# Performance work log

Measured on AMD Instinct MI355X. Metric: run time of the kernel, lower is better.

## Reference

```python
import jax, jax.numpy as jnp
import numpy as np

B, S, D = 2, 2048, 1024
H, DH = 16, 64
NEG = -1e9


def setup_inputs() -> dict:
    key = jax.random.key(0)
    ks = jax.random.split(key, 4)
    hidden_states = jax.random.normal(ks[0], (B, S, D), dtype=jnp.float32)
    # additive causal mask: 0 where allowed, -1e9 where masked
    causal = jnp.tril(jnp.ones((S, S), dtype=bool))
    attention_mask = jnp.where(causal, 0.0, NEG).astype(jnp.float32)[None, None]
    Wqkv = jax.random.normal(ks[1], (D, 3 * H * DH), dtype=jnp.float32) * (1.0 / np.sqrt(D))
    bqkv = jnp.zeros((3 * H * DH,), dtype=jnp.float32)
    Wproj = jax.random.normal(ks[2], (H * DH, D), dtype=jnp.float32) * (1.0 / np.sqrt(H * DH))
    bproj = jnp.zeros((D,), dtype=jnp.float32)
    return {"hidden_states": hidden_states, "attention_mask": attention_mask,
            "Wqkv": Wqkv, "bqkv": bqkv, "Wproj": Wproj, "bproj": bproj}


def reference(hidden_states, attention_mask, Wqkv, bqkv, Wproj, bproj):
    b, s, _ = hidden_states.shape
    scale = 1.0 / np.sqrt(DH)
    qkv = hidden_states @ Wqkv + bqkv                      # [b, s, 3*H*DH]
    q, k, v = jnp.split(qkv, 3, axis=-1)
    # [b, s, H*DH] -> [b, H, s, DH]
    def split_heads(x):
        return x.reshape(b, s, H, DH).transpose(0, 2, 1, 3)
    q, k, v = split_heads(q), split_heads(k), split_heads(v)
    scores = jnp.einsum('bhqd,bhkd->bhqk', q, k) * scale   # [b, H, s, s]
    scores = scores + attention_mask
    probs = jax.nn.softmax(scores, axis=-1)
    attn = jnp.einsum('bhqk,bhkd->bhqd', probs, v)         # [b, H, s, DH]
    attn = attn.transpose(0, 2, 1, 3).reshape(b, s, H * DH)
    out = attn @ Wproj + bproj                             # [b, s, D]
    return out
```

## Files before the change

### kernel.cpp

```cpp
#include <hip/hip_runtime.h>
#include <hip/hip_bf16.h>
#include <stdint.h>

#define B_ 2
#define S_ 2048
#define D_ 1024
#define H_ 16
#define DH_ 64
#define M_ 4096
#define LOG2E 1.44269504088896340736f

typedef __attribute__((ext_vector_type(8))) short short8;
typedef __attribute__((ext_vector_type(4))) float f32x4;
typedef __attribute__((ext_vector_type(16))) float f32x16;

__device__ __forceinline__ unsigned short f2bf(float f) {
  __hip_bfloat16 h = __float2bfloat16(f);
  union { __hip_bfloat16 h; unsigned short u; } cv;
  cv.h = h;
  return cv.u;
}

__device__ __forceinline__ unsigned int pack_bf(float lo, float hi2) {
  union { __hip_bfloat162 h; unsigned int u; } cv;
  cv.h = __float22bfloat162_rn(make_float2(lo, hi2));
  return cv.u;
}

__device__ __forceinline__ void gll16(const void* g, void* l) {
  __builtin_amdgcn_global_load_lds(
      (__attribute__((address_space(1))) void*)(g),
      (__attribute__((address_space(3))) void*)(l), 16, 0, 0);
}

__global__ __launch_bounds__(256) void k_prep(const float* __restrict__ hs,
                                              const float* __restrict__ Wqkv,
                                              const float* __restrict__ Wproj,
                                              unsigned short* __restrict__ hid,
                                              unsigned short* __restrict__ wqkvT,
                                              unsigned short* __restrict__ wprT) {
  __shared__ unsigned short tile[32][33];
  const int id = blockIdx.x;
  if (id < 4096) {
    const int i = id * 256 + threadIdx.x;
    float4 v = reinterpret_cast<const float4*>(hs)[i];
    ushort4 o;
    o.x = f2bf(v.x); o.y = f2bf(v.y); o.z = f2bf(v.z); o.w = f2bf(v.w);
    reinterpret_cast<ushort4*>(hid)[i] = o;
    return;
  }
  const float* W;
  unsigned short* WT;
  int N, i;
  if (id < 7168) { i = id - 4096; W = Wqkv; WT = wqkvT; N = 3072; }
  else           { i = id - 7168; W = Wproj; WT = wprT; N = 1024; }
  const int nb = (N == 3072) ? 96 : 32;
  const int n0 = (i % nb) * 32, k0 = (i / nb) * 32;
  const int tx = threadIdx.x & 31, ty = threadIdx.x >> 5;
#pragma unroll
  for (int j = 0; j < 4; j++) {
    int k = ty + j * 8;
    tile[k][tx] = f2bf(W[(long)(k0 + k) * N + n0 + tx]);
  }
  __syncthreads();
#pragma unroll
  for (int j = 0; j < 4; j++) {
    int n = ty + j * 8;
    WT[(long)(n0 + n) * 1024 + k0 + tx] = tile[tx][n];
  }
}

template <int MODE, int BN>
__global__ __launch_bounds__(256) void k_gemm(
    const unsigned short* __restrict__ A,
    const unsigned short* __restrict__ BT,
    const float* __restrict__ bias,
    void* __restrict__ out0,
    unsigned short* __restrict__ outk,
    unsigned short* __restrict__ outv,
    int M, int N, int K) {
  constexpr int JN = BN / 32;
  __shared__ __align__(16) unsigned short lds_a[2][128 * 32];
  __shared__ __align__(16) unsigned short lds_b[2][BN * 32];
  const int t = threadIdx.x;
  const int w = t >> 6, l = t & 63;
  const int g = l >> 4, x = l & 15;
  const int wr = w >> 1, wc = w & 1;
  const long m0 = (long)blockIdx.x * 128, n0 = (long)blockIdx.y * BN;

  f32x4 acc[4][JN];
#pragma unroll
  for (int i = 0; i < 4; i++)
#pragma unroll
    for (int j = 0; j < JN; j++) acc[i][j] = (f32x4){0.f, 0.f, 0.f, 0.f};

  const unsigned short* ga = A + (m0 + 16 * w + (l >> 2)) * (long)K + (l & 3) * 8;
  const unsigned short* gb = BT + (n0 + 16 * w + (l >> 2)) * (long)K + (l & 3) * 8;

  auto stage = [&](int nb, int k0) {
    unsigned short* la = lds_a[nb] + w * 512;
    unsigned short* lb = lds_b[nb] + w * 512;
    gll16(ga + k0, la);
    gll16(ga + k0 + 64 * (long)K, la + 2048);
    gll16(gb + k0, lb);
    if (BN == 128) gll16(gb + k0 + 64 * (long)K, lb + 2048);
  };

  stage(0, 0);
  asm volatile("s_waitcnt vmcnt(0)" ::: "memory");
  __syncthreads();

  const int nit = K >> 5;
  for (int it = 0; it < nit; it++) {
    const int cur = it & 1;
    if (it + 1 < nit) stage(cur ^ 1, (it + 1) << 5);
    short8 af[4], bfr[JN];
#pragma unroll
    for (int i = 0; i < 4; i++)
      af[i] = *reinterpret_cast<const short8*>(
          lds_a[cur] + (wr * 64 + i * 16 + x) * 32 + g * 8);
#pragma unroll
    for (int j = 0; j < JN; j++)
      bfr[j] = *reinterpret_cast<const short8*>(
          lds_b[cur] + (wc * (BN / 2) + j * 16 + x) * 32 + g * 8);
#pragma unroll
    for (int i = 0; i < 4; i++)
#pragma unroll
      for (int j = 0; j < JN; j++)
        acc[i][j] = __builtin_amdgcn_mfma_f32_16x16x32_bf16(af[i], bfr[j], acc[i][j], 0, 0, 0);
    asm volatile("s_waitcnt vmcnt(0)" ::: "memory");
    __syncthreads();
  }

#pragma unroll
  for (int i = 0; i < 4; i++) {
#pragma unroll
    for (int j = 0; j < JN; j++) {
#pragma unroll
      for (int r = 0; r < 4; r++) {
        const long m = m0 + wr * 64 + i * 16 + 4 * g + r;
        const long n = n0 + wc * (BN / 2) + j * 16 + x;
        float v = acc[i][j][r] + bias[n];
        if (MODE == 1) {
          ((float*)out0)[m * N + n] = v;
        } else {
          const int b = (int)(m >> 11), s = (int)(m & 2047);
          const int which = (int)(n >> 10);
          const int rem = (int)(n & 1023);
          const int h = rem >> 6, d = rem & 63;
          const long idx = (((long)(b * H_ + h)) * S_ + s) * DH_ + d;
          unsigned short bv = f2bf(v);
          if (which == 0) ((unsigned short*)out0)[idx] = bv;
          else if (which == 1) outk[idx] = bv;
          else outv[idx] = bv;
        }
      }
    }
  }
}

__global__ __launch_bounds__(256) void k_tr_v(const unsigned short* __restrict__ v,
                                              unsigned short* __restrict__ vt) {
  __shared__ __align__(16) unsigned short tile[64][72];
  const int bh = blockIdx.y;
  const int s0 = blockIdx.x * 64;
  const int t = threadIdx.x;
  const int r = t >> 2;
  const int c = (t & 3) * 16;
  const unsigned short* src = v + ((long)bh * S_ + s0 + r) * DH_ + c;
  *reinterpret_cast<short8*>(&tile[r][c]) = *reinterpret_cast<const short8*>(src);
  *reinterpret_cast<short8*>(&tile[r][c + 8]) = *reinterpret_cast<const short8*>(src + 8);
  __syncthreads();
  unsigned short* dst = vt + ((long)bh * DH_ + r) * S_ + s0 + c;
#pragma unroll
  for (int jj = 0; jj < 2; jj++) {
    short8 o;
#pragma unroll
    for (int j = 0; j < 8; j++) o[j] = (short)tile[c + jj * 8 + j][r];
    *reinterpret_cast<short8*>(dst + jj * 8) = o;
  }
}

__global__ __launch_bounds__(256, 1) void k_attn(const unsigned short* __restrict__ qb_,
                                                 const unsigned short* __restrict__ kb,
                                                 const unsigned short* __restrict__ vt,
                                                 unsigned short* __restrict__ attn_out) {
  __shared__ __align__(16) unsigned short lds_k[2][8192];
  __shared__ __align__(16) unsigned short lds_v[2][8192];

  const int t0_ = threadIdx.x;
  const int w = t0_ >> 6, l = t0_ & 63;
  const int q32 = l & 31, hi = l >> 5;
  const int r7 = q32 & 7;
  const int r15 = q32 & 15;
  const int lr = l >> 3, sch = (l & 7) ^ lr;
  const int lv4 = l >> 4;

  const int id = blockIdx.x;
  const int xcd = id & 7, slot = id >> 3;
  const int bh = xcd + 8 * (slot >> 4);
  const int craw = slot & 15;
  const int qc = (slot & 32) ? craw : (15 - craw);

  const int b = bh >> 4, h = bh & 15;
  const long kvbase = (long)bh * S_ * DH_;
  const long vtbase = (long)bh * DH_ * S_;
  const float SC = 0.125f * LOG2E;

  const int q0w = qc * 128 + 32 * w;
  const int qg = q0w + q32;
  const int nt = qc + 1;

  const unsigned short* kbb = kb + kvbase;
  const unsigned short* vtb = vt + vtbase;

  auto stage = [&](int nb, int kv0) {
#pragma unroll
    for (int i = 0; i < 4; i++) {
      const int R0 = 32 * w + 8 * i;
      gll16(kbb + (long)(kv0 + R0 + lr) * 64 + sch * 8, &lds_k[nb][R0 * 64]);
      const int V0 = 16 * w + 4 * i;
      const int svch = (l & 15) ^ (4 * i + lv4);
      gll16(vtb + (long)(V0 + lv4) * S_ + kv0 + svch * 8, &lds_v[nb][V0 * 128]);
    }
  };

  short8 qf[4];
#pragma unroll
  for (int f = 0; f < 4; f++)
    qf[f] = *reinterpret_cast<const short8*>(qb_ + kvbase + (long)qg * DH_ + 16 * f + 8 * hi);

  stage(0, 0);

  f32x16 oacc[2];
#pragma unroll
  for (int dt = 0; dt < 2; dt++)
#pragma unroll
    for (int r = 0; r < 16; r++) oacc[dt][r] = 0.f;
  float m = -1.0e30f, lown = 0.f;

  asm volatile("s_waitcnt vmcnt(0)" ::: "memory");
  __syncthreads();

  for (int tt = 0; tt < nt; tt++) {
    const int kv0 = tt << 7;
    if (tt + 1 < nt) stage((tt + 1) & 1, kv0 + 128);

    const unsigned short* lk = lds_k[tt & 1];
    const unsigned short* lv = lds_v[tt & 1];

    float p[64];
    const bool diag = (tt == nt - 1);
#pragma unroll
    for (int ks = 0; ks < 4; ks++) {
      f32x16 sa;
#pragma unroll
      for (int r = 0; r < 16; r++) sa[r] = 0.f;
#pragma unroll
      for (int f = 0; f < 4; f++) {
        short8 kf = *reinterpret_cast<const short8*>(
            lk + (32 * ks + q32) * 64 + (((2 * f + hi) ^ r7) << 3));
        sa = __builtin_amdgcn_mfma_f32_32x32x16_bf16(kf, qf[f], sa, 0, 0, 0);
      }
#pragma unroll
      for (int r = 0; r < 16; r++) {
        float s = sa[r] * SC;
        if (diag) {
          const int kvg = kv0 + 32 * ks + (r & 3) + 8 * (r >> 2) + 4 * hi;
          if (kvg > qg) s = -1.0e30f;
        }
        p[16 * ks + r] = s;
      }
    }

    float mx[16];
#pragma unroll
    for (int r = 0; r < 16; r++)
      mx[r] = fmaxf(fmaxf(p[r], p[r + 16]), fmaxf(p[r + 32], p[r + 48]));
#pragma unroll
    for (int st = 8; st >= 1; st >>= 1)
#pragma unroll
      for (int r = 0; r < 8; r++)
        if (r < st) mx[r] = fmaxf(mx[r], mx[r + st]);
    float pmax = fmaxf(mx[0], __shfl_xor(mx[0], 32, 64));

    if (__any(pmax > m + 8.0f)) {
      const float mn = fmaxf(m, pmax);
      const float fsc = exp2f(m - mn);
      m = mn;
      lown *= fsc;
#pragma unroll
      for (int r = 0; r < 16; r++) {
        const int rr = (r & 3) + 8 * (r >> 2) + 4 * hi;
        const float fr = __int_as_float(
            __builtin_amdgcn_ds_bpermute(rr << 2, __float_as_int(fsc)));
        oacc[0][r] *= fr;
        oacc[1][r] *= fr;
      }
    }

#pragma unroll
    for (int i = 0; i < 64; i++) p[i] = exp2f(p[i] - m);

    float sm[16];
#pragma unroll
    for (int r = 0; r < 16; r++)
      sm[r] = (p[r] + p[r + 16]) + (p[r + 32] + p[r + 48]);
#pragma unroll
    for (int st = 8; st >= 1; st >>= 1)
#pragma unroll
      for (int r = 0; r < 8; r++)
        if (r < st) sm[r] += sm[r + st];
    lown += sm[0];

#pragma unroll
    for (int s4 = 0; s4 < 8; s4++) {
      const int bse = 8 * s4;
      unsigned int t0p = pack_bf(p[bse + 0], p[bse + 1]);
      unsigned int t1p = pack_bf(p[bse + 2], p[bse + 3]);
      unsigned int t2p = pack_bf(p[bse + 4], p[bse + 5]);
      unsigned int t3p = pack_bf(p[bse + 6], p[bse + 7]);
      unsigned int s0 = hi ? t0p : t2p;
      unsigned int s1 = hi ? t1p : t3p;
      unsigned int x0 = __shfl_xor(s0, 32, 64);
      unsigned int x1 = __shfl_xor(s1, 32, 64);
      union { unsigned int u[4]; short8 s8; } pa;
      pa.u[0] = hi ? x0 : t0p;
      pa.u[1] = hi ? x1 : t1p;
      pa.u[2] = hi ? t2p : x0;
      pa.u[3] = hi ? t3p : x1;
#pragma unroll
      for (int dt = 0; dt < 2; dt++) {
        short8 vf = *reinterpret_cast<const short8*>(
            lv + (32 * dt + q32) * 128 + (((2 * s4 + hi) ^ r15) << 3));
        oacc[dt] = __builtin_amdgcn_mfma_f32_32x32x16_bf16(pa.s8, vf, oacc[dt], 0, 0, 0);
      }
    }

    asm volatile("s_waitcnt vmcnt(0)" ::: "memory");
    __syncthreads();
  }

  const float lt = lown + __shfl_xor(lown, 32, 64);
  const float linv = 1.0f / lt;
#pragma unroll
  for (int r = 0; r < 16; r++) {
    const int rr = (r & 3) + 8 * (r >> 2) + 4 * hi;
    const float li = __int_as_float(
        __builtin_amdgcn_ds_bpermute(rr << 2, __float_as_int(linv)));
    const long row = (long)b * S_ + q0w + rr;
#pragma unroll
    for (int dt = 0; dt < 2; dt++)
      attn_out[row * (H_ * DH_) + h * DH_ + 32 * dt + q32] = f2bf(oacc[dt][r] * li);
  }
}

extern "C" void kernel_launch(void* const* d_in, const int* in_sizes, int n_in,
                              void* d_out, int out_size, void* d_ws, size_t ws_size,
                              hipStream_t stream) {
  (void)in_sizes; (void)n_in; (void)out_size; (void)ws_size;
  const float* hs    = (const float*)d_in[0];
  const float* Wqkv  = (const float*)d_in[2];
  const float* bqkv  = (const float*)d_in[3];
  const float* Wproj = (const float*)d_in[4];
  const float* bproj = (const float*)d_in[5];
  float* out = (float*)d_out;

  unsigned short* ws    = (unsigned short*)d_ws;
  unsigned short* hid   = ws;
  unsigned short* wqkvT = hid + 4194304;
  unsigned short* wprT  = wqkvT + 3145728;
  unsigned short* q_b   = wprT + 1048576;
  unsigned short* k_b   = q_b + 4194304;
  unsigned short* v_b   = k_b + 4194304;
  unsigned short* vt_b  = v_b + 4194304;
  unsigned short* ao    = vt_b + 4194304;

  k_prep<<<8192, 256, 0, stream>>>(hs, Wqkv, Wproj, hid, wqkvT, wprT);
  k_gemm<0, 128><<<dim3(32, 24), 256, 0, stream>>>(hid, wqkvT, bqkv, (void*)q_b, k_b, v_b,
                                                   4096, 3072, 1024);
  k_tr_v<<<dim3(32, 32), 256, 0, stream>>>(v_b, vt_b);
  k_attn<<<512, 256, 0, stream>>>(q_b, k_b, vt_b, ao);
  k_gemm<1, 64><<<dim3(32, 16), 256, 0, stream>>>(ao, wprT, bproj, (void*)out, nullptr, nullptr,
                                                  4096, 1024, 1024);
}
```

Measured before the change: 212.8 us.

## Split attention KV range across two wave groups and pair causal chunks per block

The attention kernel now uses 512-thread blocks where two 4-wave groups each process alternating KV tiles for the same 128-query chunk, then merge their partial softmax states through LDS. Each block handles a pair of query chunks (pr and 15-pr) so every block gets equal causal work, and the grid shrinks to 256 blocks. This aims to fix load imbalance from the causal triangle and add parallelism within a chunk. In exchange it costs extra LDS, a combine step with bf16-rounded partial outputs, and more barriers.

```diff
diff --git a/kernel.cpp b/kernel.cpp
--- a/kernel.cpp
+++ b/kernel.cpp
@@ -19,6 +19,10 @@
   union { __hip_bfloat16 h; unsigned short u; } cv;
   cv.h = h;
   return cv.u;
+}
+
+__device__ __forceinline__ float bf2f(unsigned short u) {
+  union { uint32_t u; float f; } x; x.u = (uint32_t)u << 16; return x.f;
 }
 
 __device__ __forceinline__ unsigned int pack_bf(float lo, float hi2) {
@@ -181,177 +185,214 @@
   }
 }
 
-__global__ __launch_bounds__(256, 1) void k_attn(const unsigned short* __restrict__ qb_,
+__global__ __launch_bounds__(512, 2) void k_attn(const unsigned short* __restrict__ qb_,
                                                  const unsigned short* __restrict__ kb,
                                                  const unsigned short* __restrict__ vt,
                                                  unsigned short* __restrict__ attn_out) {
-  __shared__ __align__(16) unsigned short lds_k[2][8192];
-  __shared__ __align__(16) unsigned short lds_v[2][8192];
+  __shared__ __align__(16) unsigned short lds_k[2][2][8192];
+  __shared__ __align__(16) unsigned short lds_v[2][2][8192];
+  __shared__ float cmb_m[256], cmb_l[256];
+  __shared__ unsigned int cmb_o[256][16];
 
   const int t0_ = threadIdx.x;
-  const int w = t0_ >> 6, l = t0_ & 63;
+  const int w = t0_ >> 6;
+  const int grp = w >> 2, wi = w & 3;
+  const int l = t0_ & 63;
   const int q32 = l & 31, hi = l >> 5;
   const int r7 = q32 & 7;
   const int r15 = q32 & 15;
   const int lr = l >> 3, sch = (l & 7) ^ lr;
   const int lv4 = l >> 4;
+  const int slot = wi * 64 + l;
 
   const int id = blockIdx.x;
-  const int xcd = id & 7, slot = id >> 3;
-  const int bh = xcd + 8 * (slot >> 4);
-  const int craw = slot & 15;
-  const int qc = (slot & 32) ? craw : (15 - craw);
+  const int xcd = id & 7, sl2 = id >> 3;
+  const int bh = 4 * xcd + (sl2 & 3);
+  const int pr = sl2 >> 2;
 
   const int b = bh >> 4, h = bh & 15;
   const long kvbase = (long)bh * S_ * DH_;
   const long vtbase = (long)bh * DH_ * S_;
   const float SC = 0.125f * LOG2E;
 
-  const int q0w = qc * 128 + 32 * w;
-  const int qg = q0w + q32;
-  const int nt = qc + 1;
-
   const unsigned short* kbb = kb + kvbase;
   const unsigned short* vtb = vt + vtbase;
 
-  auto stage = [&](int nb, int kv0) {
+  auto stage = [&](int buf, int kv0) {
 #pragma unroll
     for (int i = 0; i < 4; i++) {
-      const int R0 = 32 * w + 8 * i;
-      gll16(kbb + (long)(kv0 + R0 + lr) * 64 + sch * 8, &lds_k[nb][R0 * 64]);
-      const int V0 = 16 * w + 4 * i;
+      const int R0 = 32 * wi + 8 * i;
+      gll16(kbb + (long)(kv0 + R0 + lr) * 64 + sch * 8, &lds_k[grp][buf][R0 * 64]);
+      const int V0 = 16 * wi + 4 * i;
       const int svch = (l & 15) ^ (4 * i + lv4);
-      gll16(vtb + (long)(V0 + lv4) * S_ + kv0 + svch * 8, &lds_v[nb][V0 * 128]);
+      gll16(vtb + (long)(V0 + lv4) * S_ + kv0 + svch * 8, &lds_v[grp][buf][V0 * 128]);
     }
   };
 
-  short8 qf[4];
-#pragma unroll
-  for (int f = 0; f < 4; f++)
-    qf[f] = *reinterpret_cast<const short8*>(qb_ + kvbase + (long)qg * DH_ + 16 * f + 8 * hi);
-
-  stage(0, 0);
-
-  f32x16 oacc[2];
-#pragma unroll
-  for (int dt = 0; dt < 2; dt++)
-#pragma unroll
-    for (int r = 0; r < 16; r++) oacc[dt][r] = 0.f;
-  float m = -1.0e30f, lown = 0.f;
-
-  asm volatile("s_waitcnt vmcnt(0)" ::: "memory");
-  __syncthreads();
-
-  for (int tt = 0; tt < nt; tt++) {
-    const int kv0 = tt << 7;
-    if (tt + 1 < nt) stage((tt + 1) & 1, kv0 + 128);
-
-    const unsigned short* lk = lds_k[tt & 1];
-    const unsigned short* lv = lds_v[tt & 1];
-
-    float p[64];
-    const bool diag = (tt == nt - 1);
-#pragma unroll
-    for (int ks = 0; ks < 4; ks++) {
-      f32x16 sa;
-#pragma unroll
-      for (int r = 0; r < 16; r++) sa[r] = 0.f;
-#pragma unroll
-      for (int f = 0; f < 4; f++) {
-        short8 kf = *reinterpret_cast<const short8*>(
-            lk + (32 * ks + q32) * 64 + (((2 * f + hi) ^ r7) << 3));
-        sa = __builtin_amdgcn_mfma_f32_32x32x16_bf16(kf, qf[f], sa, 0, 0, 0);
+#pragma unroll 1
+  for (int ch = 0; ch < 2; ch++) {
+    const int qc = ch ? (15 - pr) : pr;
+    const int ntot = qc + 1;
+    const int N = (ntot + 1) >> 1;
+    const int ng = (ntot + (grp == 0 ? 1 : 0)) >> 1;
+
+    const int q0w = qc * 128 + 32 * wi;
+    const int qg = q0w + q32;
+
+    short8 qf[4];
+#pragma unroll
+    for (int f = 0; f < 4; f++)
+      qf[f] = *reinterpret_cast<const short8*>(
+          qb_ + kvbase + (long)qg * DH_ + 16 * f + 8 * hi);
+
+    f32x16 oacc[2];
+#pragma unroll
+    for (int dt = 0; dt < 2; dt++)
+#pragma unroll
+      for (int r = 0; r < 16; r++) oacc[dt][r] = 0.f;
+    float m = -1.0e30f, lown = 0.f;
+
+    if (ng > 0) stage(0, grp << 7);
+    asm volatile("s_waitcnt vmcnt(0)" ::: "memory");
+    __syncthreads();
+
+    for (int s = 0; s < N; s++) {
+      const int tile = grp + 2 * s;
+      if (s + 1 < ng) stage((s + 1) & 1, (grp + 2 * (s + 1)) << 7);
+      if (s < ng) {
+        const int kv0 = tile << 7;
+        const unsigned short* lk = lds_k[grp][s & 1];
+        const unsigned short* lv = lds_v[grp][s & 1];
+        const bool diag = (tile == qc);
+
+        float p[64];
+#pragma unroll
+        for (int ks = 0; ks < 4; ks++) {
+          f32x16 sa;
+#pragma unroll
+          for (int r = 0; r < 16; r++) sa[r] = 0.f;
+#pragma unroll
+          for (int f = 0; f < 4; f++) {
+            short8 kf = *reinterpret_cast<const short8*>(
+                lk + (32 * ks + q32) * 64 + (((2 * f + hi) ^ r7) << 3));
+            sa = __builtin_amdgcn_mfma_f32_32x32x16_bf16(kf, qf[f], sa, 0, 0, 0);
+          }
+#pragma unroll
+          for (int r = 0; r < 16; r++) {
+            float s2 = sa[r] * SC;
+            if (diag) {
+              const int kvg = kv0 + 32 * ks + (r & 3) + 8 * (r >> 2) + 4 * hi;
+              if (kvg > qg) s2 = -1.0e30f;
+            }
+            p[16 * ks + r] = s2;
+          }
+        }
+
+        float mx[16];
+#pragma unroll
+        for (int r = 0; r < 16; r++)
+          mx[r] = fmaxf(fmaxf(p[r], p[r + 16]), fmaxf(p[r + 32], p[r + 48]));
+#pragma unroll
+        for (int st = 8; st >= 1; st >>= 1)
+#pragma unroll
+          for (int r = 0; r < 8; r++)
+            if (r < st) mx[r] = fmaxf(mx[r], mx[r + st]);
+        float pmax = fmaxf(mx[0], __shfl_xor(mx[0], 32, 64));
+
+        if (__any(pmax > m + 8.0f)) {
+          const float mn = fmaxf(m, pmax);
+          const float fsc = exp2f(m - mn);
+          m = mn;
+          lown *= fsc;
+#pragma unroll
+          for (int r = 0; r < 16; r++) {
+            const int rr = (r & 3) + 8 * (r >> 2) + 4 * hi;
+            const float fr = __int_as_float(
+                __builtin_amdgcn_ds_bpermute(rr << 2, __float_as_int(fsc)));
+            oacc[0][r] *= fr;
+            oacc[1][r] *= fr;
+          }
+        }
+
+#pragma unroll
+        for (int i = 0; i < 64; i++) p[i] = exp2f(p[i] - m);
+
+        float sm[16];
+#pragma unroll
+        for (int r = 0; r < 16; r++)
+          sm[r] = (p[r] + p[r + 16]) + (p[r + 32] + p[r + 48]);
+#pragma unroll
+        for (int st = 8; st >= 1; st >>= 1)
+#pragma unroll
+          for (int r = 0; r < 8; r++)
+            if (r < st) sm[r] += sm[r + st];
+        lown += sm[0];
+
+#pragma unroll
+        for (int s4 = 0; s4 < 8; s4++) {
+          const int bse = 8 * s4;
+          unsigned int t0p = pack_bf(p[bse + 0], p[bse + 1]);
+          unsigned int t1p = pack_bf(p[bse + 2], p[bse + 3]);
+          unsigned int t2p = pack_bf(p[bse + 4], p[bse + 5]);
+          unsigned int t3p = pack_bf(p[bse + 6], p[bse + 7]);
+          unsigned int s0 = hi ? t0p : t2p;
+          unsigned int s1 = hi ? t1p : t3p;
+          unsigned int x0 = __shfl_xor(s0, 32, 64);
+          unsigned int x1 = __shfl_xor(s1, 32, 64);
+          union { unsigned int u[4]; short8 s8; } pa;
+          pa.u[0] = hi ? x0 : t0p;
+          pa.u[1] = hi ? x1 : t1p;
+          pa.u[2] = hi ? t2p : x0;
+          pa.u[3] = hi ? t3p : x1;
+#pragma unroll
+          for (int dt = 0; dt < 2; dt++) {
+            short8 vf = *reinterpret_cast<const short8*>(
+                lv + (32 * dt + q32) * 128 + (((2 * s4 + hi) ^ r15) << 3));
+            oacc[dt] = __builtin_amdgcn_mfma_f32_32x32x16_bf16(pa.s8, vf, oacc[dt], 0, 0, 0);
+          }
+        }
       }
+      asm volatile("s_waitcnt vmcnt(0)" ::: "memory");
+      __syncthreads();
+    }
+
+    if (grp == 1) {
+      const float lt1 = lown + __shfl_xor(lown, 32, 64);
+      cmb_m[slot] = m;
+      cmb_l[slot] = lt1;
+#pragma unroll
+      for (int dt = 0; dt < 2; dt++)
+#pragma unroll
+        for (int i = 0; i < 8; i++)
+          cmb_o[slot][dt * 8 + i] = pack_bf(oacc[dt][2 * i], oacc[dt][2 * i + 1]);
+    }
+    __syncthreads();
+    if (grp == 0) {
+      const float lt0 = lown + __shfl_xor(lown, 32, 64);
+      const float m1 = cmb_m[slot], l1c = cmb_l[slot];
+      const float ms = fmaxf(m, m1);
+      const float w0 = exp2f(m - ms), w1 = exp2f(m1 - ms);
+      const float linv = 1.0f / (w0 * lt0 + w1 * l1c);
 #pragma unroll
       for (int r = 0; r < 16; r++) {
-        float s = sa[r] * SC;
-        if (diag) {
-          const int kvg = kv0 + 32 * ks + (r & 3) + 8 * (r >> 2) + 4 * hi;
-          if (kvg > qg) s = -1.0e30f;
+        const int rr = (r & 3) + 8 * (r >> 2) + 4 * hi;
+        const float w0r = __int_as_float(
+            __builtin_amdgcn_ds_bpermute(rr << 2, __float_as_int(w0)));
+        const float w1r = __int_as_float(
+            __builtin_amdgcn_ds_bpermute(rr << 2, __float_as_int(w1)));
+        const float lir = __int_as_float(
+            __builtin_amdgcn_ds_bpermute(rr << 2, __float_as_int(linv)));
+        const long row = (long)b * S_ + q0w + rr;
+#pragma unroll
+        for (int dt = 0; dt < 2; dt++) {
+          const unsigned int wd = cmb_o[slot][dt * 8 + (r >> 1)];
+          const float o1 = bf2f((unsigned short)((r & 1) ? (wd >> 16) : (wd & 0xffffu)));
+          attn_out[row * (H_ * DH_) + h * DH_ + 32 * dt + q32] =
+              f2bf((w0r * oacc[dt][r] + w1r * o1) * lir);
         }
-        p[16 * ks + r] = s;
       }
     }
-
-    float mx[16];
-#pragma unroll
-    for (int r = 0; r < 16; r++)
-      mx[r] = fmaxf(fmaxf(p[r], p[r + 16]), fmaxf(p[r + 32], p[r + 48]));
-#pragma unroll
-    for (int st = 8; st >= 1; st >>= 1)
-#pragma unroll
-      for (int r = 0; r < 8; r++)
-        if (r < st) mx[r] = fmaxf(mx[r], mx[r + st]);
-    float pmax = fmaxf(mx[0], __shfl_xor(mx[0], 32, 64));
-
-    if (__any(pmax > m + 8.0f)) {
-      const float mn = fmaxf(m, pmax);
-      const float fsc = exp2f(m - mn);
-      m = mn;
-      lown *= fsc;
-#pragma unroll
-      for (int r = 0; r < 16; r++) {
-        const int rr = (r & 3) + 8 * (r >> 2) + 4 * hi;
-        const float fr = __int_as_float(
-            __builtin_amdgcn_ds_bpermute(rr << 2, __float_as_int(fsc)));
-        oacc[0][r] *= fr;
-        oacc[1][r] *= fr;
-      }
-    }
-
-#pragma unroll
-    for (int i = 0; i < 64; i++) p[i] = exp2f(p[i] - m);
-
-    float sm[16];
-#pragma unroll
-    for (int r = 0; r < 16; r++)
-      sm[r] = (p[r] + p[r + 16]) + (p[r + 32] + p[r + 48]);
-#pragma unroll
-    for (int st = 8; st >= 1; st >>= 1)
-#pragma unroll
-      for (int r = 0; r < 8; r++)
-        if (r < st) sm[r] += sm[r + st];
-    lown += sm[0];
-
-#pragma unroll
-    for (int s4 = 0; s4 < 8; s4++) {
-      const int bse = 8 * s4;
-      unsigned int t0p = pack_bf(p[bse + 0], p[bse + 1]);
-      unsigned int t1p = pack_bf(p[bse + 2], p[bse + 3]);
-      unsigned int t2p = pack_bf(p[bse + 4], p[bse + 5]);
-      unsigned int t3p = pack_bf(p[bse + 6], p[bse + 7]);
-      unsigned int s0 = hi ? t0p : t2p;
-      unsigned int s1 = hi ? t1p : t3p;
-      unsigned int x0 = __shfl_xor(s0, 32, 64);
-      unsigned int x1 = __shfl_xor(s1, 32, 64);
-      union { unsigned int u[4]; short8 s8; } pa;
-      pa.u[0] = hi ? x0 : t0p;
-      pa.u[1] = hi ? x1 : t1p;
-      pa.u[2] = hi ? t2p : x0;
-      pa.u[3] = hi ? t3p : x1;
-#pragma unroll
-      for (int dt = 0; dt < 2; dt++) {
-        short8 vf = *reinterpret_cast<const short8*>(
-            lv + (32 * dt + q32) * 128 + (((2 * s4 + hi) ^ r15) << 3));
-        oacc[dt] = __builtin_amdgcn_mfma_f32_32x32x16_bf16(pa.s8, vf, oacc[dt], 0, 0, 0);
-      }
-    }
-
-    asm volatile("s_waitcnt vmcnt(0)" ::: "memory");
     __syncthreads();
-  }
-
-  const float lt = lown + __shfl_xor(lown, 32, 64);
-  const float linv = 1.0f / lt;
-#pragma unroll
-  for (int r = 0; r < 16; r++) {
-    const int rr = (r & 3) + 8 * (r >> 2) + 4 * hi;
-    const float li = __int_as_float(
-        __builtin_amdgcn_ds_bpermute(rr << 2, __float_as_int(linv)));
-    const long row = (long)b * S_ + q0w + rr;
-#pragma unroll
-    for (int dt = 0; dt < 2; dt++)
-      attn_out[row * (H_ * DH_) + h * DH_ + 32 * dt + q32] = f2bf(oacc[dt][r] * li);
   }
 }
 
@@ -380,7 +421,7 @@
   k_gemm<0, 128><<<dim3(32, 24), 256, 0, stream>>>(hid, wqkvT, bqkv, (void*)q_b, k_b, v_b,
                                                    4096, 3072, 1024);
   k_tr_v<<<dim3(32, 32), 256, 0, stream>>>(v_b, vt_b);
-  k_attn<<<512, 256, 0, stream>>>(q_b, k_b, vt_b, ao);
+  k_attn<<<256, 512, 0, stream>>>(q_b, k_b, vt_b, ao);
   k_gemm<1, 64><<<dim3(32, 16), 256, 0, stream>>>(ao, wprT, bproj, (void*)out, nullptr, nullptr,
                                                   4096, 1024, 1024);
 }
```

New measurement: 202.6 us. 1.05x faster.
